# Kernel tuning notes

Hardware: AMD Instinct MI355X
Metric: run time of the kernel (lower is better)

## Reference

```python
import jax, jax.numpy as jnp
import numpy as np

N_BINS = 1024
N_DIFFS = 16777216
EPS = 1e-4  # denominator stabilizer from the original code


def setup_inputs() -> dict:
    key = jax.random.key(0)
    k1, k2 = jax.random.split(key)
    # bin centers are probabilities strictly inside (0,1) so logit is finite
    bin_centers = jax.random.uniform(k1, (N_BINS,), dtype=jnp.float32,
                                     minval=0.01, maxval=0.99)
    observation_probability_index = jax.random.randint(
        k2, (N_DIFFS, 3), 0, N_BINS, dtype=jnp.int64
    ) if jax.config.jax_enable_x64 else jax.random.randint(
        k2, (N_DIFFS, 3), 0, N_BINS, dtype=jnp.int32)
    # 6 scalar bound parameters (lower_bound_{1,2,3}=-10, upper_bound_{1,2,3}=10)
    lb = jnp.full((3,), -10.0, dtype=jnp.float32)
    ub = jnp.full((3,), 10.0, dtype=jnp.float32)
    return {
        "bin_centers": bin_centers,
        "observation_probability_index": observation_probability_index,
        "lb": lb,
        "ub": ub,
        "operator_number": 2,
    }


def reference(bin_centers, observation_probability_index, lb, ub, operator_number):
    # operator_number only selects which (single) parameter dict is used in the
    # original module; the math is identical, so it is unused here.
    c = bin_centers[observation_probability_index]          # [n_diffs, 3] gather
    logit = jnp.log(c / (1.0 - c))                          # math.log(t/(1-t))
    x = (ub - logit) / (ub - lb + EPS)                      # broadcast over rows
    return jnp.prod(jax.nn.sigmoid(x), axis=-1)             # [n_diffs]
```

## Files before the change

### kernel.cpp

```cpp
#include <hip/hip_runtime.h>
#include <math.h>

#define N_BINS_MAX 1024
#define EPS 1e-4f

__global__ __launch_bounds__(256) void pm_kernel(
    const float* __restrict__ bin_centers, int n_bins,
    const int* __restrict__ idx,
    const float* __restrict__ lb,
    const float* __restrict__ ub,
    float* __restrict__ out,
    long long n_rows)
{
    __shared__ float tab0[N_BINS_MAX];
    __shared__ float tab1[N_BINS_MAX];
    __shared__ float tab2[N_BINS_MAX];

    const float lb0 = lb[0], lb1 = lb[1], lb2 = lb[2];
    const float ub0 = ub[0], ub1 = ub[1], ub2 = ub[2];
    const float r0 = 1.0f / (ub0 - lb0 + EPS);
    const float r1 = 1.0f / (ub1 - lb1 + EPS);
    const float r2 = 1.0f / (ub2 - lb2 + EPS);

    for (int i = threadIdx.x; i < n_bins; i += blockDim.x) {
        float c = bin_centers[i];
        float logit = logf(c / (1.0f - c));
        float x0 = (ub0 - logit) * r0;
        float x1 = (ub1 - logit) * r1;
        float x2 = (ub2 - logit) * r2;
        tab0[i] = 1.0f / (1.0f + expf(-x0));
        tab1[i] = 1.0f / (1.0f + expf(-x1));
        tab2[i] = 1.0f / (1.0f + expf(-x2));
    }
    __syncthreads();

    const long long n_quads = n_rows >> 2;
    const int4* __restrict__ idx4 = (const int4*)idx;
    float4* __restrict__ out4 = (float4*)out;
    const long long stride = (long long)gridDim.x * blockDim.x;

    #pragma unroll 2
    for (long long q = (long long)blockIdx.x * blockDim.x + threadIdx.x;
         q < n_quads; q += stride) {
        int4 a = idx4[3 * q + 0];
        int4 b = idx4[3 * q + 1];
        int4 c = idx4[3 * q + 2];
        float4 r;
        r.x = tab0[a.x] * tab1[a.y] * tab2[a.z];
        r.y = tab0[a.w] * tab1[b.x] * tab2[b.y];
        r.z = tab0[b.z] * tab1[b.w] * tab2[c.x];
        r.w = tab0[c.y] * tab1[c.z] * tab2[c.w];
        out4[q] = r;
    }

    const long long tail_start = n_quads << 2;
    for (long long row = tail_start + (long long)blockIdx.x * blockDim.x + threadIdx.x;
         row < n_rows; row += stride) {
        int i0 = idx[3 * row + 0];
        int i1 = idx[3 * row + 1];
        int i2 = idx[3 * row + 2];
        out[row] = tab0[i0] * tab1[i1] * tab2[i2];
    }
}

extern "C" void kernel_launch(void* const* d_in, const int* in_sizes, int n_in,
                              void* d_out, int out_size, void* d_ws, size_t ws_size,
                              hipStream_t stream) {
    const float* bin_centers = (const float*)d_in[0];
    const int*   idx         = (const int*)d_in[1];
    const float* lb          = (const float*)d_in[2];
    const float* ub          = (const float*)d_in[3];
    float* out = (float*)d_out;

    int n_bins = in_sizes[0];
    long long n_rows = (long long)in_sizes[1] / 3;

    const int block = 256;
    long long n_quads = n_rows >> 2;
    long long want = (n_quads + block - 1) / block;
    if (want < 1) want = 1;
    int grid = (int)((want > 2048) ? 2048 : want);

    pm_kernel<<<grid, block, 0, stream>>>(bin_centers, n_bins, idx, lb, ub, out, n_rows);
}
```

Before: 308.0 us.

## Coalesce index loads via per-wave LDS transpose with register prefetch

Each wave now loads a 64-quad chunk of indices as contiguous int4 vectors, so lanes read adjacent addresses instead of stride-3 int4s. It then transposes them through a per-wave LDS staging buffer into per-row layout. The next chunk's indices are prefetched into registers while the current one is processed. Block size rises to 512 and the grid is sized by chunks. The costs are extra LDS traffic and possible bank conflicts from the staging writes, plus reliance on wave-level ordering with only a compiler barrier instead of a real sync.

```diff
diff --git a/kernel.cpp b/kernel.cpp
--- a/kernel.cpp
+++ b/kernel.cpp
@@ -3,8 +3,10 @@
 
 #define N_BINS_MAX 1024
 #define EPS 1e-4f
+#define BLOCK 512
+#define WPB (BLOCK / 64)
 
-__global__ __launch_bounds__(256) void pm_kernel(
+__global__ __launch_bounds__(BLOCK) void pm_kernel(
     const float* __restrict__ bin_centers, int n_bins,
     const int* __restrict__ idx,
     const float* __restrict__ lb,
@@ -15,6 +17,7 @@
     __shared__ float tab0[N_BINS_MAX];
     __shared__ float tab1[N_BINS_MAX];
     __shared__ float tab2[N_BINS_MAX];
+    __shared__ int4 stg[WPB][3][64];
 
     const float lb0 = lb[0], lb1 = lb[1], lb2 = lb[2];
     const float ub0 = ub[0], ub1 = ub[1], ub2 = ub[2];
@@ -34,14 +37,61 @@
     }
     __syncthreads();
 
+    const int lane = threadIdx.x & 63;
+    const int wid  = threadIdx.x >> 6;
+
+    int d_[3], k_[3];
+    #pragma unroll
+    for (int j = 0; j < 3; ++j) {
+        int f = j * 64 + lane;
+        d_[j] = f / 3;
+        k_[j] = f - 3 * d_[j];
+    }
+
     const long long n_quads = n_rows >> 2;
+    const long long nchunk  = n_quads >> 6;
     const int4* __restrict__ idx4 = (const int4*)idx;
     float4* __restrict__ out4 = (float4*)out;
-    const long long stride = (long long)gridDim.x * blockDim.x;
 
-    #pragma unroll 2
-    for (long long q = (long long)blockIdx.x * blockDim.x + threadIdx.x;
-         q < n_quads; q += stride) {
+    const long long gws = (long long)gridDim.x * WPB;
+    long long ch = (long long)blockIdx.x * WPB + wid;
+
+    if (ch < nchunk) {
+        long long f4 = 3 * (ch << 6);
+        int4 v0 = idx4[f4 + lane];
+        int4 v1 = idx4[f4 + 64 + lane];
+        int4 v2 = idx4[f4 + 128 + lane];
+        for (;;) {
+            const long long cur = ch;
+            int4 a0 = v0, a1 = v1, a2 = v2;
+            ch += gws;
+            if (ch < nchunk) {
+                long long nf4 = 3 * (ch << 6);
+                v0 = idx4[nf4 + lane];
+                v1 = idx4[nf4 + 64 + lane];
+                v2 = idx4[nf4 + 128 + lane];
+            }
+            stg[wid][k_[0]][d_[0]] = a0;
+            stg[wid][k_[1]][d_[1]] = a1;
+            stg[wid][k_[2]][d_[2]] = a2;
+            asm volatile("" ::: "memory");
+            int4 a = stg[wid][0][lane];
+            int4 b = stg[wid][1][lane];
+            int4 c = stg[wid][2][lane];
+            float4 r;
+            r.x = tab0[a.x] * tab1[a.y] * tab2[a.z];
+            r.y = tab0[a.w] * tab1[b.x] * tab2[b.y];
+            r.z = tab0[b.z] * tab1[b.w] * tab2[c.x];
+            r.w = tab0[c.y] * tab1[c.z] * tab2[c.w];
+            out4[(cur << 6) + lane] = r;
+            if (ch >= nchunk) break;
+        }
+    }
+
+    const long long done_quads = nchunk << 6;
+    const long long tid = (long long)blockIdx.x * BLOCK + threadIdx.x;
+    const long long tstride = (long long)gridDim.x * BLOCK;
+    for (long long q = done_quads + tid; q < n_quads; q += tstride) {
         int4 a = idx4[3 * q + 0];
         int4 b = idx4[3 * q + 1];
         int4 c = idx4[3 * q + 2];
@@ -54,8 +104,7 @@
     }
 
     const long long tail_start = n_quads << 2;
-    for (long long row = tail_start + (long long)blockIdx.x * blockDim.x + threadIdx.x;
-         row < n_rows; row += stride) {
+    for (long long row = tail_start + tid; row < n_rows; row += tstride) {
         int i0 = idx[3 * row + 0];
         int i1 = idx[3 * row + 1];
         int i2 = idx[3 * row + 2];
@@ -75,11 +124,11 @@
     int n_bins = in_sizes[0];
     long long n_rows = (long long)in_sizes[1] / 3;
 
-    const int block = 256;
     long long n_quads = n_rows >> 2;
-    long long want = (n_quads + block - 1) / block;
+    long long nchunk  = n_quads >> 6;
+    long long want = (nchunk + WPB - 1) / WPB;
     if (want < 1) want = 1;
     int grid = (int)((want > 2048) ? 2048 : want);
 
-    pm_kernel<<<grid, block, 0, stream>>>(bin_centers, n_bins, idx, lb, ub, out, n_rows);
+    pm_kernel<<<grid, BLOCK, 0, stream>>>(bin_centers, n_bins, idx, lb, ub, out, n_rows);
 }
```

New measurement: 304.1 us. No clear change (-1.3%).
